# Performance work log

Measured on AMD Instinct MI355X. Metric: run time of the kernel, lower is better.

## Reference

```python
import jax, jax.numpy as jnp
import numpy as np

EMB = 1024
HEADS = 16
HEAD_DIM = EMB // HEADS


def setup_inputs() -> dict:
    key = jax.random.key(0)
    ks = jax.random.split(key, 9)
    B, T = 2, 2048
    s = 1.0 / np.sqrt(EMB)
    x = jax.random.normal(ks[0], (B, T, EMB), dtype=jnp.float32)
    Wq = jax.random.normal(ks[1], (EMB, EMB), dtype=jnp.float32) * s
    bq = jnp.zeros((EMB,), dtype=jnp.float32)
    Wk = jax.random.normal(ks[2], (EMB, EMB), dtype=jnp.float32) * s
    bk = jnp.zeros((EMB,), dtype=jnp.float32)
    Wv = jax.random.normal(ks[3], (EMB, EMB), dtype=jnp.float32) * s
    bv = jnp.zeros((EMB,), dtype=jnp.float32)
    Wo = jax.random.normal(ks[4], (EMB, EMB), dtype=jnp.float32) * s
    bo = jnp.zeros((EMB,), dtype=jnp.float32)
    return {"x": x, "Wq": Wq, "bq": bq, "Wk": Wk, "bk": bk,
            "Wv": Wv, "bv": bv, "Wo": Wo, "bo": bo}


def reference(x, Wq, bq, Wk, bk, Wv, bv, Wo, bo):
    B, T, C = x.shape
    H, D = HEADS, HEAD_DIM
    # QKV projections -> (B, H, T, D)
    q = (x @ Wq + bq).reshape(B, T, H, D).transpose(0, 2, 1, 3)
    k = (x @ Wk + bk).reshape(B, T, H, D).transpose(0, 2, 1, 3)
    v = (x @ Wv + bv).reshape(B, T, H, D).transpose(0, 2, 1, 3)
    scores = jnp.einsum('bhqd,bhkd->bhqk', q, k) / np.sqrt(D).astype(np.float32)
    causal = jnp.tril(jnp.ones((T, T), dtype=bool))  # True where allowed
    scores = jnp.where(causal, scores, -jnp.inf)
    weights = jax.nn.softmax(scores, axis=-1)  # dropout is identity at eval
    out = jnp.einsum('bhqk,bhkd->bhqd', weights, v)
    out = out.transpose(0, 2, 1, 3).reshape(B, T, C)
    return out @ Wo + bo
```

## Files before the change

### kernel.cpp

```cpp
#include <hip/hip_runtime.h>

typedef unsigned short u16;
typedef u16 u16x8 __attribute__((ext_vector_type(8)));
typedef __bf16 bf16x8 __attribute__((ext_vector_type(8)));
typedef float f32x4 __attribute__((ext_vector_type(4)));

#define EMB 1024
#define TT 2048
#define BB 2
#define NHEADS 16
#define HD 64
#define MTOT (BB * TT)

__device__ __forceinline__ u16 cvt(float f) {
  return __builtin_bit_cast(u16, (__bf16)f);
}

__device__ __forceinline__ bf16x8 asbf(u16x8 v) {
  return __builtin_bit_cast(bf16x8, v);
}

__device__ __forceinline__ void gload16(const void* g, void* l) {
  __builtin_amdgcn_global_load_lds(
      (const __attribute__((address_space(1))) void*)g,
      (__attribute__((address_space(3))) void*)l, 16, 0, 0);
}

__global__ __launch_bounds__(256) void k_prep(
    const float* __restrict__ x, u16* __restrict__ xb,
    const float* __restrict__ W0, const float* __restrict__ W1,
    const float* __restrict__ W2, const float* __restrict__ W3,
    u16* __restrict__ T0, u16* __restrict__ T1, u16* __restrict__ T2,
    u16* __restrict__ T3) {
  __shared__ float tile[32][33];
  const int bid = blockIdx.x;
  const int tid = threadIdx.x;
  if (bid >= 4096) {
    int i = (bid - 4096) * 256 + tid;
    float4 a = ((const float4*)x)[i * 2];
    float4 b = ((const float4*)x)[i * 2 + 1];
    u16x8 o;
    o[0] = cvt(a.x); o[1] = cvt(a.y); o[2] = cvt(a.z); o[3] = cvt(a.w);
    o[4] = cvt(b.x); o[5] = cvt(b.y); o[6] = cvt(b.z); o[7] = cvt(b.w);
    ((u16x8*)xb)[i] = o;
    return;
  }
  const int z = bid >> 10;
  const float* __restrict__ W = (z == 0) ? W0 : (z == 1) ? W1 : (z == 2) ? W2 : W3;
  u16* __restrict__ Wt = (z == 0) ? T0 : (z == 1) ? T1 : (z == 2) ? T2 : T3;
  const int b = bid & 1023;
  const int bx = (b & 31) * 32, by = (b >> 5) * 32;
  const int tx = tid & 31;
  const int ty = tid >> 5;
#pragma unroll
  for (int r = ty; r < 32; r += 8) tile[r][tx] = W[(by + r) * EMB + bx + tx];
  __syncthreads();
  const int tx2 = tid & 15;
  const int ty2 = tid >> 4;
#pragma unroll
  for (int r = ty2; r < 32; r += 16) {
    unsigned v = (unsigned)cvt(tile[2 * tx2][r]) |
                 ((unsigned)cvt(tile[2 * tx2 + 1][r]) << 16);
    *(unsigned*)&Wt[(bx + r) * EMB + by + 2 * tx2] = v;
  }
}

__global__ __launch_bounds__(256) void k_gemm_qkv(
    const u16* __restrict__ xb, const u16* __restrict__ WqT,
    const u16* __restrict__ WkT, const u16* __restrict__ WvT,
    const float* __restrict__ bq, const float* __restrict__ bk,
    const float* __restrict__ bv, u16* __restrict__ Q, u16* __restrict__ K,
    u16* __restrict__ Vt) {
  __shared__ u16 Al[128 * 64];
  __shared__ u16 Bl[128 * 64];
  const int tid = threadIdx.x;
  const int lane = tid & 63;
  const int w = tid >> 6;
  const int wr = w >> 1, wc = w & 1;
  const int lr = lane & 15, lg = lane >> 4;
  const int m0 = blockIdx.x * 128;
  const int nb = blockIdx.y;
  const int seg = nb >> 3;
  const int n0 = (nb & 7) * 128;
  const u16* __restrict__ Bt = (seg == 0) ? WqT : (seg == 1) ? WkT : WvT;
  const float* __restrict__ bias = (seg == 0) ? bq : (seg == 1) ? bk : bv;

  f32x4 acc[4][4];
#pragma unroll
  for (int i = 0; i < 4; i++)
#pragma unroll
    for (int j = 0; j < 4; j++) acc[i][j] = (f32x4){0.f, 0.f, 0.f, 0.f};

  const int srow = tid >> 3;
  const int sgz = ((tid >> 3) & 3) | (((tid >> 6) & 1) << 2);
  const int sc = (tid & 7) ^ sgz;
  const u16* ga0 = xb + (m0 + srow) * EMB + sc * 8;
  const u16* gb0 = Bt + (n0 + srow) * EMB + sc * 8;
  char* la0 = (char*)Al + w * 1024;
  char* lb0 = (char*)Bl + w * 1024;
  const int gfr = (lr & 3) | (((lr >> 3) & 1) << 2);

  for (int k0 = 0; k0 < EMB; k0 += 64) {
#pragma unroll
    for (int m = 0; m < 4; m++) {
      gload16(ga0 + (32 * m) * EMB + k0, la0 + m * 4096);
      gload16(gb0 + (32 * m) * EMB + k0, lb0 + m * 4096);
    }
    __syncthreads();
    u16x8 af[4][2], bfr[4][2];
#pragma unroll
    for (int hh = 0; hh < 2; hh++) {
      const int pc = ((hh * 4 + lg) ^ gfr) * 16;
#pragma unroll
      for (int mi = 0; mi < 4; mi++)
        af[mi][hh] =
            *(const u16x8*)((char*)Al + (wr * 64 + mi * 16 + lr) * 128 + pc);
#pragma unroll
      for (int ni = 0; ni < 4; ni++)
        bfr[ni][hh] =
            *(const u16x8*)((char*)Bl + (wc * 64 + ni * 16 + lr) * 128 + pc);
    }
#pragma unroll
    for (int hh = 0; hh < 2; hh++)
#pragma unroll
      for (int mi = 0; mi < 4; mi++)
#pragma unroll
        for (int ni = 0; ni < 4; ni++)
          acc[mi][ni] = __builtin_amdgcn_mfma_f32_16x16x32_bf16(
              asbf(af[mi][hh]), asbf(bfr[ni][hh]), acc[mi][ni], 0, 0, 0);
    __syncthreads();
  }

#pragma unroll
  for (int mi = 0; mi < 4; mi++) {
    const int lmb = wr * 64 + mi * 16 + lg * 4;
#pragma unroll
    for (int ni = 0; ni < 4; ni++) {
      const int ln = wc * 64 + ni * 16 + lr;
      const int n = n0 + ln;
      const float bv_ = bias[n];
      const int h = n >> 6, d = n & 63;
#pragma unroll
      for (int r = 0; r < 4; r++) {
        const int m = m0 + lmb + r;
        const int b = m >> 11, t = m & 2047;
        float v = acc[mi][ni][r] + bv_;
        if (seg == 0) {
          v *= 0.18033688011f;
          Q[(((b * NHEADS + h) * TT) + t) * HD + d] = cvt(v);
        } else if (seg == 1) {
          K[(((b * NHEADS + h) * TT) + t) * HD + d] = cvt(v);
        } else {
          Vt[(((b * NHEADS + h) * HD) + d) * TT + t] = cvt(v);
        }
      }
    }
  }
}

__global__ __launch_bounds__(256) void k_attn(const u16* __restrict__ Q,
                                              const u16* __restrict__ Kg,
                                              const u16* __restrict__ Vt,
                                              u16* __restrict__ AO) {
  __shared__ u16 Kl[2][64 * 64];
  __shared__ u16 Vl[2][64 * 64];
  const int tid = threadIdx.x;
  const int lane = tid & 63;
  const int w = tid >> 6;
  const int lr = lane & 15, lg = lane >> 4;
  const int bh = blockIdx.x;
  const int pair = blockIdx.y;
  const int lo = pair, hi = 63 - pair;
  const int b32 = (w < 2) ? hi : lo;
  const int myend = b32 >> 1;
  const int q0 = b32 * 32 + (w & 1) * 16;
  const u16* __restrict__ Qh = Q + bh * TT * HD;
  const u16* __restrict__ Kh = Kg + bh * TT * HD;
  const u16* __restrict__ Vh = Vt + bh * HD * TT;

  const int srow = tid >> 3;
  const int sgz = ((tid >> 3) & 3) | (((tid >> 6) & 1) << 2);
  const int sc = (tid & 7) ^ sgz;

  u16x8 qf[2];
  qf[0] = *(const u16x8*)&Qh[(q0 + lr) * HD + lg * 8];
  qf[1] = *(const u16x8*)&Qh[(q0 + lr) * HD + 32 + lg * 8];

  f32x4 accO[4];
#pragma unroll
  for (int i = 0; i < 4; i++) accO[i] = (f32x4){0.f, 0.f, 0.f, 0.f};
  float mst = -__builtin_inff();
  float lsum = 0.f;

  const int nkt = (hi >> 1) + 1;

  gload16(Kh + srow * HD + sc * 8, (char*)Kl[0] + w * 1024);
  gload16(Kh + (srow + 32) * HD + sc * 8, (char*)Kl[0] + w * 1024 + 4096);
  gload16(Vh + srow * TT + sc * 8, (char*)Vl[0] + w * 1024);
  gload16(Vh + (srow + 32) * TT + sc * 8, (char*)Vl[0] + w * 1024 + 4096);
  __syncthreads();

  for (int kt = 0; kt < nkt; ++kt) {
    const int k0 = kt * 64;
    const int cur = kt & 1;
    if (kt + 1 < nkt) {
      const int kn = k0 + 64;
      char* kd = (char*)Kl[cur ^ 1] + w * 1024;
      char* vd = (char*)Vl[cur ^ 1] + w * 1024;
      gload16(Kh + (kn + srow) * HD + sc * 8, kd);
      gload16(Kh + (kn + srow + 32) * HD + sc * 8, kd + 4096);
      gload16(Vh + srow * TT + kn + sc * 8, vd);
      gload16(Vh + (srow + 32) * TT + kn + sc * 8, vd + 4096);
    }
    if (kt <= myend) {
      const char* Kc = (const char*)Kl[cur];
      const char* Vc = (const char*)Vl[cur];

      f32x4 s[4];
#pragma unroll
      for (int n = 0; n < 4; n++) s[n] = (f32x4){0.f, 0.f, 0.f, 0.f};
      __builtin_amdgcn_s_setprio(1);
#pragma unroll
      for (int n = 0; n < 4; n++) {
        const int kr =
            (lr & 3) + ((n & 1) << 2) + ((lr >> 2) << 3) + ((n >> 1) << 5);
        const int gg = (kr & 3) | (((kr >> 3) & 1) << 2);
#pragma unroll
        for (int dh = 0; dh < 2; dh++) {
          const int bo = ((dh * 4 + lg) ^ gg) << 4;
          u16x8 kf = *(const u16x8*)(Kc + kr * 128 + bo);
          s[n] = __builtin_amdgcn_mfma_f32_16x16x32_bf16(asbf(kf), asbf(qf[dh]),
                                                         s[n], 0, 0, 0);
        }
      }
      __builtin_amdgcn_s_setprio(0);
      if (kt == myend) {
        const int rowq = q0 + lr;
#pragma unroll
        for (int n = 0; n < 4; n++) {
          const int cb = k0 + ((n & 1) << 2) + (lg << 3) + ((n >> 1) << 5);
#pragma unroll
          for (int r = 0; r < 4; r++)
            if (cb + r > rowq) s[n][r] = -__builtin_inff();
        }
      }
      float m01 = fmaxf(fmaxf(s[0][0], s[0][1]), fmaxf(s[0][2], s[0][3]));
      float m1 = fmaxf(fmaxf(s[1][0], s[1][1]), fmaxf(s[1][2], s[1][3]));
      float m2 = fmaxf(fmaxf(s[2][0], s[2][1]), fmaxf(s[2][2], s[2][3]));
      float m3 = fmaxf(fmaxf(s[3][0], s[3][1]), fmaxf(s[3][2], s[3][3]));
      float lmax = fmaxf(fmaxf(m01, m1), fmaxf(m2, m3));
      if (!__all(lmax - mst <= 11.0f)) {
        float rm = lmax;
        rm = fmaxf(rm, __shfl_xor(rm, 16));
        rm = fmaxf(rm, __shfl_xor(rm, 32));
        float mnew = fmaxf(mst, rm);
        float corr = exp2f(mst - mnew);
        lsum *= corr;
        mst = mnew;
#pragma unroll
        for (int r = 0; r < 4; r++) {
          float ca = __shfl(corr, 20 * lg + r);
#pragma unroll
          for (int dt = 0; dt < 4; dt++) accO[dt][r] *= ca;
        }
      }
      float p[4][4];
      float ls = 0.f;
#pragma unroll
      for (int n = 0; n < 4; n++)
#pragma unroll
        for (int r = 0; r < 4; r++) {
          p[n][r] = exp2f(s[n][r] - mst);
          ls += p[n][r];
        }
      lsum += ls;
      u16x8 a1, a2;
#pragma unroll
      for (int r = 0; r < 4; r++) {
        a1[r] = cvt(p[0][r]);
        a1[4 + r] = cvt(p[1][r]);
        a2[r] = cvt(p[2][r]);
        a2[4 + r] = cvt(p[3][r]);
      }
      __builtin_amdgcn_s_setprio(1);
#pragma unroll
      for (int dt = 0; dt < 4; dt++) {
        const int row = dt * 16 + lr;
        const int gg = (row & 3) | (((row >> 3) & 1) << 2);
        const int bo0 = ((lg ^ gg) << 4);
        const int bo1 = (((4 + lg) ^ gg) << 4);
        u16x8 vf0 = *(const u16x8*)(Vc + row * 128 + bo0);
        u16x8 vf1 = *(const u16x8*)(Vc + row * 128 + bo1);
        accO[dt] = __builtin_amdgcn_mfma_f32_16x16x32_bf16(asbf(a1), asbf(vf0),
                                                           accO[dt], 0, 0, 0);
        accO[dt] = __builtin_amdgcn_mfma_f32_16x16x32_bf16(asbf(a2), asbf(vf1),
                                                           accO[dt], 0, 0, 0);
      }
      __builtin_amdgcn_s_setprio(0);
    }
    __syncthreads();
  }
  float t = lsum;
  t += __shfl_xor(t, 16);
  t += __shfl_xor(t, 32);
  float rinv = 1.0f / t;
  float ra[4];
#pragma unroll
  for (int r = 0; r < 4; r++) ra[r] = __shfl(rinv, 20 * lg + r);
  const int b = bh >> 4, h = bh & 15;
#pragma unroll
  for (int dt = 0; dt < 4; dt++)
#pragma unroll
    for (int r = 0; r < 4; r++) {
      const int row = q0 + lg * 4 + r;
      const int d = h * 64 + dt * 16 + lr;
      AO[(b * TT + row) * EMB + d] = cvt(accO[dt][r] * ra[r]);
    }
}

__global__ __launch_bounds__(256) void k_gemm_out(const u16* __restrict__ AO,
                                                  const u16* __restrict__ WoT,
                                                  const float* __restrict__ bo,
                                                  float* __restrict__ out) {
  __shared__ u16 Al[128 * 64];
  __shared__ u16 Bl[128 * 64];
  const int tid = threadIdx.x;
  const int lane = tid & 63;
  const int w = tid >> 6;
  const int wr = w >> 1, wc = w & 1;
  const int lr = lane & 15, lg = lane >> 4;
  const int m0 = blockIdx.x * 128;
  const int n0 = blockIdx.y * 128;

  f32x4 acc[4][4];
#pragma unroll
  for (int i = 0; i < 4; i++)
#pragma unroll
    for (int j = 0; j < 4; j++) acc[i][j] = (f32x4){0.f, 0.f, 0.f, 0.f};

  const int srow = tid >> 3;
  const int sgz = ((tid >> 3) & 3) | (((tid >> 6) & 1) << 2);
  const int sc = (tid & 7) ^ sgz;
  const u16* ga0 = AO + (m0 + srow) * EMB + sc * 8;
  const u16* gb0 = WoT + (n0 + srow) * EMB + sc * 8;
  char* la0 = (char*)Al + w * 1024;
  char* lb0 = (char*)Bl + w * 1024;
  const int gfr = (lr & 3) | (((lr >> 3) & 1) << 2);

  for (int k0 = 0; k0 < EMB; k0 += 64) {
#pragma unroll
    for (int m = 0; m < 4; m++) {
      gload16(ga0 + (32 * m) * EMB + k0, la0 + m * 4096);
      gload16(gb0 + (32 * m) * EMB + k0, lb0 + m * 4096);
    }
    __syncthreads();
    u16x8 af[4][2], bfr[4][2];
#pragma unroll
    for (int hh = 0; hh < 2; hh++) {
      const int pc = ((hh * 4 + lg) ^ gfr) * 16;
#pragma unroll
      for (int mi = 0; mi < 4; mi++)
        af[mi][hh] =
            *(const u16x8*)((char*)Al + (wr * 64 + mi * 16 + lr) * 128 + pc);
#pragma unroll
      for (int ni = 0; ni < 4; ni++)
        bfr[ni][hh] =
            *(const u16x8*)((char*)Bl + (wc * 64 + ni * 16 + lr) * 128 + pc);
    }
#pragma unroll
    for (int hh = 0; hh < 2; hh++)
#pragma unroll
      for (int mi = 0; mi < 4; mi++)
#pragma unroll
        for (int ni = 0; ni < 4; ni++)
          acc[mi][ni] = __builtin_amdgcn_mfma_f32_16x16x32_bf16(
              asbf(af[mi][hh]), asbf(bfr[ni][hh]), acc[mi][ni], 0, 0, 0);
    __syncthreads();
  }

#pragma unroll
  for (int mi = 0; mi < 4; mi++) {
    const int lmb = wr * 64 + mi * 16 + lg * 4;
#pragma unroll
    for (int ni = 0; ni < 4; ni++) {
      const int ln = wc * 64 + ni * 16 + lr;
      const int n = n0 + ln;
      const float bv_ = bo[n];
#pragma unroll
      for (int r = 0; r < 4; r++) {
        const int m = m0 + lmb + r;
        out[m * EMB + n] = acc[mi][ni][r] + bv_;
      }
    }
  }
}

extern "C" void kernel_launch(void* const* d_in, const int* in_sizes, int n_in,
                              void* d_out, int out_size, void* d_ws,
                              size_t ws_size, hipStream_t stream) {
  const float* x = (const float*)d_in[0];
  const float* Wq = (const float*)d_in[1];
  const float* bq = (const float*)d_in[2];
  const float* Wk = (const float*)d_in[3];
  const float* bk = (const float*)d_in[4];
  const float* Wv = (const float*)d_in[5];
  const float* bv = (const float*)d_in[6];
  const float* Wo = (const float*)d_in[7];
  const float* bo = (const float*)d_in[8];
  float* out = (float*)d_out;

  char* ws = (char*)d_ws;
  u16* xb = (u16*)ws;
  u16* WqT = (u16*)(ws + (8u << 20));
  u16* WkT = (u16*)(ws + (10u << 20));
  u16* WvT = (u16*)(ws + (12u << 20));
  u16* WoT = (u16*)(ws + (14u << 20));
  u16* Qb = (u16*)(ws + (16u << 20));
  u16* Kb = (u16*)(ws + (24u << 20));
  u16* Vtb = (u16*)(ws + (32u << 20));
  u16* AO = xb;

  k_prep<<<6144, 256, 0, stream>>>(x, xb, Wq, Wk, Wv, Wo, WqT, WkT, WvT, WoT);
  k_gemm_qkv<<<dim3(32, 24), 256, 0, stream>>>(xb, WqT, WkT, WvT, bq, bk, bv,
                                               Qb, Kb, Vtb);
  k_attn<<<dim3(32, 32), 256, 0, stream>>>(Qb, Kb, Vtb, AO);
  k_gemm_out<<<dim3(32, 8), 256, 0, stream>>>(AO, WoT, bo, out);
}
```

Measured before the change: 130.4 us.

## Use 512-thread attention blocks with triple-buffered K/V prefetch and one barrier

The attention kernel now runs eight waves per block, each pair of 64-row query blocks (low and high causal halves) sharing the K/V tiles, so the grid shrinks from 32x32 to 32x16 blocks. K/V staging moves from double to triple buffering, prefetching two tiles ahead with explicit vmcnt waits and a single barrier per iteration in place of two syncthreads. This is meant to reduce global traffic per query row and hide load latency better. In exchange it uses more LDS per block and relies on hand-written waitcnt counts, and fewer, larger blocks could leave some compute units with uneven load.

```diff
diff --git a/kernel.cpp b/kernel.cpp
--- a/kernel.cpp
+++ b/kernel.cpp
@@ -158,22 +158,22 @@
   }
 }
 
-__global__ __launch_bounds__(256) void k_attn(const u16* __restrict__ Q,
+__global__ __launch_bounds__(512) void k_attn(const u16* __restrict__ Q,
                                               const u16* __restrict__ Kg,
                                               const u16* __restrict__ Vt,
                                               u16* __restrict__ AO) {
-  __shared__ u16 Kl[2][64 * 64];
-  __shared__ u16 Vl[2][64 * 64];
+  __shared__ u16 Kl[3][64 * 64];
+  __shared__ u16 Vl[3][64 * 64];
   const int tid = threadIdx.x;
   const int lane = tid & 63;
   const int w = tid >> 6;
   const int lr = lane & 15, lg = lane >> 4;
   const int bh = blockIdx.x;
   const int pair = blockIdx.y;
-  const int lo = pair, hi = 63 - pair;
-  const int b32 = (w < 2) ? hi : lo;
-  const int myend = b32 >> 1;
-  const int q0 = b32 * 32 + (w & 1) * 16;
+  const int lo = pair, hi = 31 - pair;
+  const int qblk = (w < 4) ? hi : lo;
+  const int myend = qblk;
+  const int q0 = qblk * 64 + (w & 3) * 16;
   const u16* __restrict__ Qh = Q + bh * TT * HD;
   const u16* __restrict__ Kh = Kg + bh * TT * HD;
   const u16* __restrict__ Vh = Vt + bh * HD * TT;
@@ -192,29 +192,30 @@
   float mst = -__builtin_inff();
   float lsum = 0.f;
 
-  const int nkt = (hi >> 1) + 1;
+  const int nkt = hi + 1;
 
   gload16(Kh + srow * HD + sc * 8, (char*)Kl[0] + w * 1024);
-  gload16(Kh + (srow + 32) * HD + sc * 8, (char*)Kl[0] + w * 1024 + 4096);
   gload16(Vh + srow * TT + sc * 8, (char*)Vl[0] + w * 1024);
-  gload16(Vh + (srow + 32) * TT + sc * 8, (char*)Vl[0] + w * 1024 + 4096);
-  __syncthreads();
+  gload16(Kh + (64 + srow) * HD + sc * 8, (char*)Kl[1] + w * 1024);
+  gload16(Vh + srow * TT + 64 + sc * 8, (char*)Vl[1] + w * 1024);
 
   for (int kt = 0; kt < nkt; ++kt) {
     const int k0 = kt * 64;
-    const int cur = kt & 1;
-    if (kt + 1 < nkt) {
-      const int kn = k0 + 64;
-      char* kd = (char*)Kl[cur ^ 1] + w * 1024;
-      char* vd = (char*)Vl[cur ^ 1] + w * 1024;
-      gload16(Kh + (kn + srow) * HD + sc * 8, kd);
-      gload16(Kh + (kn + srow + 32) * HD + sc * 8, kd + 4096);
-      gload16(Vh + srow * TT + kn + sc * 8, vd);
-      gload16(Vh + (srow + 32) * TT + kn + sc * 8, vd + 4096);
+    if (kt == nkt - 1)
+      asm volatile("s_waitcnt vmcnt(0)" ::: "memory");
+    else
+      asm volatile("s_waitcnt vmcnt(2)" ::: "memory");
+    __builtin_amdgcn_s_barrier();
+    __builtin_amdgcn_sched_barrier(0);
+    if (kt + 2 < nkt) {
+      const int kn = k0 + 128;
+      const int bn = (kt + 2) % 3;
+      gload16(Kh + (kn + srow) * HD + sc * 8, (char*)Kl[bn] + w * 1024);
+      gload16(Vh + srow * TT + kn + sc * 8, (char*)Vl[bn] + w * 1024);
     }
     if (kt <= myend) {
-      const char* Kc = (const char*)Kl[cur];
-      const char* Vc = (const char*)Vl[cur];
+      const char* Kc = (const char*)Kl[kt % 3];
+      const char* Vc = (const char*)Vl[kt % 3];
 
       f32x4 s[4];
 #pragma unroll
@@ -298,7 +299,6 @@
       }
       __builtin_amdgcn_s_setprio(0);
     }
-    __syncthreads();
   }
   float t = lsum;
   t += __shfl_xor(t, 16);
@@ -423,6 +423,6 @@
   k_prep<<<6144, 256, 0, stream>>>(x, xb, Wq, Wk, Wv, Wo, WqT, WkT, WvT, WoT);
   k_gemm_qkv<<<dim3(32, 24), 256, 0, stream>>>(xb, WqT, WkT, WvT, bq, bk, bv,
                                                Qb, Kb, Vtb);
-  k_attn<<<dim3(32, 32), 256, 0, stream>>>(Qb, Kb, Vtb, AO);
+  k_attn<<<dim3(32, 16), 512, 0, stream>>>(Qb, Kb, Vtb, AO);
   k_gemm_out<<<dim3(32, 8), 256, 0, stream>>>(AO, WoT, bo, out);
 }
```

Result: faster. 118.5 us (-9.1%).
